# Optimization experiments

Hardware: AMD Instinct MI355X
Metric: run time of the kernel (lower is better)

Reference implementation:

```python
import jax, jax.numpy as jnp
import numpy as np
import math

D_MODEL = 1024
N_HEAD = 16
D_HEAD = D_MODEL // N_HEAD  # 64
D_KMAP = 128
B, L = 4, 4096


def setup_inputs() -> dict:
    key = jax.random.key(0)
    ks = jax.random.split(key, 10)
    s = 1.0 / math.sqrt(D_MODEL)
    inp = {
        "x": jax.random.normal(ks[0], (B, L, D_MODEL), dtype=jnp.float32),
        "proj_mat": jax.random.normal(ks[1], (D_HEAD, D_KMAP), dtype=jnp.float32),
        "Wq": jax.random.uniform(ks[2], (D_MODEL, D_MODEL), minval=-s, maxval=s),
        "bq": jax.random.uniform(ks[3], (D_MODEL,), minval=-s, maxval=s),
        "Wk": jax.random.uniform(ks[4], (D_MODEL, D_MODEL), minval=-s, maxval=s),
        "bk": jax.random.uniform(ks[5], (D_MODEL,), minval=-s, maxval=s),
        "Wv": jax.random.uniform(ks[6], (D_MODEL, D_MODEL), minval=-s, maxval=s),
        "bv": jax.random.uniform(ks[7], (D_MODEL,), minval=-s, maxval=s),
        "Wo": jax.random.uniform(ks[8], (D_MODEL, D_MODEL), minval=-s, maxval=s),
        "bo": jax.random.uniform(ks[9], (D_MODEL,), minval=-s, maxval=s),
    }
    return inp


def _fourier_kernel(x, proj_mat):
    # x: [B,L,H,d_head] -> [B,L,H,2*d_kmap]
    p = jnp.einsum("blhd,dm->blhm", x, proj_mat) / math.sqrt(D_HEAD)
    return jnp.concatenate([jnp.cos(p), jnp.sin(p)], axis=-1) / math.sqrt(D_KMAP)


def reference(x, proj_mat, Wq, bq, Wk, bk, Wv, bv, Wo, bo):
    Bv, Lv, _ = x.shape
    q = (x @ Wq.T + bq).reshape(Bv, Lv, N_HEAD, D_HEAD)
    k = (x @ Wk.T + bk).reshape(Bv, Lv, N_HEAD, D_HEAD)
    v = (x @ Wv.T + bv).reshape(Bv, Lv, N_HEAD, D_HEAD)
    q_prime = _fourier_kernel(q, proj_mat)  # [B,L,H,2M]
    k_prime = _fourier_kernel(k, proj_mat)  # [B,L,H,2M]
    kv = jnp.einsum("blhm,blhd->bhmd", k_prime, v)  # [B,H,2M,d_head]
    out = jnp.einsum("blhm,bhmd->blhd", q_prime, kv)  # [B,L,H,d_head]
    out = out.reshape(Bv, Lv, D_MODEL)
    return out @ Wo.T + bo
```

## Files before the change

kernel.cpp:

```cpp
#include <hip/hip_runtime.h>
#include <cstddef>
#include <cstdint>


typedef __attribute__((ext_vector_type(8))) short s8v;
typedef __attribute__((ext_vector_type(4))) short s4v;
typedef __attribute__((ext_vector_type(4))) float f32x4;

#define MFMA_BF16(a, b, c) __builtin_amdgcn_mfma_f32_16x16x32_bf16((a), (b), (c), 0, 0, 0)

#define P_SCALE 0.125f
#define F_SCALE 0.08838834764831845f

static __device__ __forceinline__ unsigned short f2bf(float f) {
  unsigned int u = __float_as_uint(f);
  u += 0x7fffu + ((u >> 16) & 1u);
  return (unsigned short)(u >> 16);
}

static __device__ __forceinline__ void gload_lds16(const void* g, void* l) {
  __builtin_amdgcn_global_load_lds(
      (const __attribute__((address_space(1))) unsigned int*)g,
      (__attribute__((address_space(3))) unsigned int*)l, 16, 0, 0);
}

__global__ void conv_all_kernel(const float* __restrict__ x,
                                const float* __restrict__ Wq, const float* __restrict__ Wk,
                                const float* __restrict__ Wv, const float* __restrict__ Wo,
                                const float* __restrict__ proj,
                                short* __restrict__ xb, short* __restrict__ Wqkvb,
                                short* __restrict__ Wob, short* __restrict__ projT) {
  const int bid = blockIdx.x;
  const int t = threadIdx.x;
  if (bid < 16384) {
    int i4 = (bid * 256 + t) * 4;
    float4 f = *(const float4*)(x + i4);
    s4v v;
    v[0] = (short)f2bf(f.x); v[1] = (short)f2bf(f.y);
    v[2] = (short)f2bf(f.z); v[3] = (short)f2bf(f.w);
    *(s4v*)(xb + i4) = v;
  } else if (bid < 20480) {
    int wi = (bid - 16384) >> 10;
    int lb = (bid - 16384) & 1023;
    const float* src = (wi == 0) ? Wq : (wi == 1) ? Wk : (wi == 2) ? Wv : Wo;
    short* dst = (wi < 3) ? (Wqkvb + (size_t)wi * 1048576) : Wob;
    int i4 = (lb * 256 + t) * 4;
    float4 f = *(const float4*)(src + i4);
    s4v v;
    v[0] = (short)f2bf(f.x); v[1] = (short)f2bf(f.y);
    v[2] = (short)f2bf(f.z); v[3] = (short)f2bf(f.w);
    *(s4v*)(dst + i4) = v;
  } else {
#pragma unroll
    for (int i = 0; i < 32; ++i) {
      int idx = t + i * 256;
      int d = idx >> 7, m = idx & 127;
      projT[m * 64 + d] = (short)f2bf(proj[idx]);
    }
  }
}

__global__ void qkv_gemm_kernel(const short* __restrict__ xb,
                                const short* __restrict__ Wqkv,
                                const float* __restrict__ bq_, const float* __restrict__ bk_,
                                const float* __restrict__ bv_,
                                short* __restrict__ qb, short* __restrict__ kb,
                                short* __restrict__ vT) {
  __shared__ __align__(16) short smem[17408];
  short* Al = smem;
  short* Bl = smem + 8192;

  const int t = threadIdx.x;
  const int bm = blockIdx.x, bn = blockIdx.y;
  const int row0 = bm * 128, n0 = bn * 128;
  const int lane = t & 63, w = t >> 6;
  const int wm = w & 1, wn = w >> 1;
  const int l15 = lane & 15, lq = lane >> 4;
  const int sx = (l15 & 7) * 8;

  f32x4 acc[4][4];
#pragma unroll
  for (int i = 0; i < 4; ++i)
#pragma unroll
    for (int j = 0; j < 4; ++j) acc[i][j] = (f32x4){0.f, 0.f, 0.f, 0.f};

  for (int k0 = 0; k0 < 1024; k0 += 64) {
#pragma unroll
    for (int i = 0; i < 4; ++i) {
      int c = t + i * 256;
      int r = c >> 3, cl = c & 7;
      int cg = cl ^ (r & 7);
      gload_lds16(xb   + (size_t)(row0 + r) * 1024 + k0 + cg * 8, Al + c * 8);
      gload_lds16(Wqkv + (size_t)(n0 + r) * 1024 + k0 + cg * 8, Bl + c * 8);
    }
    __syncthreads();
#pragma unroll
    for (int ks = 0; ks < 2; ++ks) {
      const int kb8 = (ks * 4 + lq) * 8;
      s8v af[4], bfr[4];
#pragma unroll
      for (int i = 0; i < 4; ++i)
        af[i] = *(s8v*)&Al[(wm * 64 + i * 16 + l15) * 64 + (kb8 ^ sx)];
#pragma unroll
      for (int j = 0; j < 4; ++j)
        bfr[j] = *(s8v*)&Bl[(wn * 64 + j * 16 + l15) * 64 + (kb8 ^ sx)];
#pragma unroll
      for (int i = 0; i < 4; ++i)
#pragma unroll
        for (int j = 0; j < 4; ++j)
          acc[i][j] = MFMA_BF16(af[i], bfr[j], acc[i][j]);
    }
    __syncthreads();
  }

  const int region = bn >> 3;
  if (region < 2) {
    const float* bias = (region == 0) ? bq_ : bk_;
    short* IM = smem;
#pragma unroll
    for (int j = 0; j < 4; ++j) {
      int cl = wn * 64 + j * 16 + l15;
      float bsv = bias[(n0 & 1023) + cl];
#pragma unroll
      for (int i = 0; i < 4; ++i)
#pragma unroll
        for (int r = 0; r < 4; ++r)
          IM[(wm * 64 + i * 16 + lq * 4 + r) * 136 + cl] = (short)f2bf(acc[i][j][r] + bsv);
    }
    __syncthreads();
    short* dst = (region == 0) ? qb : kb;
#pragma unroll
    for (int i = 0; i < 8; ++i) {
      int c = t + i * 256;
      int r = c >> 4, cc = c & 15;
      *(s8v*)&dst[(size_t)(row0 + r) * 1024 + (n0 & 1023) + cc * 8] =
          *(s8v*)&IM[r * 136 + cc * 8];
    }
  } else {
    short* IM = smem;
#pragma unroll
    for (int j = 0; j < 4; ++j) {
      int cl = wn * 64 + j * 16 + l15;
      float bsv = bv_[(n0 - 2048) + cl];
#pragma unroll
      for (int i = 0; i < 4; ++i) {
        s4v pk;
#pragma unroll
        for (int r = 0; r < 4; ++r) pk[r] = (short)f2bf(acc[i][j][r] + bsv);
        *(s4v*)&IM[cl * 136 + wm * 64 + i * 16 + lq * 4] = pk;
      }
    }
    __syncthreads();
    const int b = row0 >> 12;
    const int l0 = (bm & 31) * 128;
#pragma unroll
    for (int i = 0; i < 8; ++i) {
      int c = t + i * 256;
      int ci = c >> 4, cc = c & 15;
      int cv = (bn - 16) * 128 + ci;
      int grow = (b * 16 + (cv >> 6)) * 64 + (cv & 63);
      *(s8v*)&vT[(size_t)grow * 4096 + l0 + cc * 8] = *(s8v*)&IM[ci * 136 + cc * 8];
    }
  }
}

__global__ void kv_accum_kernel(const short* __restrict__ kb, const short* __restrict__ vT,
                                const short* __restrict__ projT, float* __restrict__ kv) {
  __shared__ __align__(16) short smem[26624];
  short* kt = smem;
  short* vt = smem + 4096;
  short* kpT = smem + 8192;

  const int t = threadIdx.x;
  const int bid = blockIdx.x;
  const int chunk = bid & 7, h = (bid >> 3) & 15, b = bid >> 7;
  const int lane = t & 63, w = t >> 6;
  const int l15 = lane & 15, lq = lane >> 4;
  const int sx = (l15 & 7) * 8;

  s8v pf[8][2];
#pragma unroll
  for (int nt = 0; nt < 8; ++nt)
#pragma unroll
    for (int ks = 0; ks < 2; ++ks)
      pf[nt][ks] = *(const s8v*)(projT + (size_t)(nt * 16 + l15) * 64 + ks * 32 + lq * 8);

  f32x4 kvacc[4][4];
#pragma unroll
  for (int i = 0; i < 4; ++i)
#pragma unroll
    for (int j = 0; j < 4; ++j) kvacc[i][j] = (f32x4){0.f, 0.f, 0.f, 0.f};

  for (int s = 0; s < 8; ++s) {
    const int l0s = chunk * 512 + s * 64;
#pragma unroll
    for (int i = 0; i < 2; ++i) {
      int c = t + i * 256;
      int r = c >> 3, cl = c & 7;
      int cg = cl ^ (r & 7);
      gload_lds16(kb + (size_t)(b * 4096 + l0s + r) * 1024 + h * 64 + cg * 8, kt + c * 8);
      gload_lds16(vT + (size_t)((b * 16 + h) * 64 + r) * 4096 + l0s + cg * 8, vt + c * 8);
    }
    __syncthreads();

    f32x4 pacc[8];
#pragma unroll
    for (int nt = 0; nt < 8; ++nt) pacc[nt] = (f32x4){0.f, 0.f, 0.f, 0.f};
#pragma unroll
    for (int ks = 0; ks < 2; ++ks) {
      const int kb8 = (ks * 4 + lq) * 8;
      s8v af = *(s8v*)&kt[(w * 16 + l15) * 64 + (kb8 ^ sx)];
#pragma unroll
      for (int nt = 0; nt < 8; ++nt) pacc[nt] = MFMA_BF16(af, pf[nt][ks], pacc[nt]);
    }
#pragma unroll
    for (int nt = 0; nt < 8; ++nt) {
      s4v cp, sp;
#pragma unroll
      for (int r = 0; r < 4; ++r) {
        float p = pacc[nt][r] * P_SCALE;
        float sv, cv;
        __sincosf(p, &sv, &cv);
        cp[r] = (short)f2bf(cv * F_SCALE);
        sp[r] = (short)f2bf(sv * F_SCALE);
      }
      int m = nt * 16 + l15;
      int rbase = w * 16 + lq * 4;
      *(s4v*)&kpT[m * 72 + rbase] = cp;
      *(s4v*)&kpT[(m + 128) * 72 + rbase] = sp;
    }
    __syncthreads();

#pragma unroll
    for (int ks = 0; ks < 2; ++ks) {
      const int kb8 = (ks * 4 + lq) * 8;
      s8v af[4], bf4[4];
#pragma unroll
      for (int i = 0; i < 4; ++i)
        af[i] = *(s8v*)&kpT[(w * 64 + i * 16 + l15) * 72 + ks * 32 + lq * 8];
#pragma unroll
      for (int j = 0; j < 4; ++j)
        bf4[j] = *(s8v*)&vt[(j * 16 + l15) * 64 + (kb8 ^ sx)];
#pragma unroll
      for (int i = 0; i < 4; ++i)
#pragma unroll
        for (int j = 0; j < 4; ++j)
          kvacc[i][j] = MFMA_BF16(af[i], bf4[j], kvacc[i][j]);
    }
    __syncthreads();
  }

  float* kvb = kv + (size_t)chunk * 1048576 + ((size_t)(b * 16 + h) << 14);
#pragma unroll
  for (int i = 0; i < 4; ++i)
#pragma unroll
    for (int j = 0; j < 4; ++j)
#pragma unroll
      for (int r = 0; r < 4; ++r) {
        int m = w * 64 + i * 16 + lq * 4 + r;
        int d = j * 16 + l15;
        kvb[(size_t)m * 64 + d] = kvacc[i][j][r];
      }
}

__global__ void kvT_kernel(const float* __restrict__ kvp, short* __restrict__ kvT) {
  __shared__ __align__(16) short im[4608];
  const int t = threadIdx.x;
  const int bh = blockIdx.x, mc = blockIdx.y;
  const float* base = kvp + (size_t)bh * 16384 + (size_t)mc * 4096;
#pragma unroll
  for (int i = 0; i < 4; ++i) {
    int idx4 = t + i * 256;
    int mm = idx4 >> 4, d4 = (idx4 & 15) * 4;
    float4 s = {0.f, 0.f, 0.f, 0.f};
#pragma unroll
    for (int c = 0; c < 8; ++c) {
      float4 v = *(const float4*)(base + (size_t)c * 1048576 + mm * 64 + d4);
      s.x += v.x; s.y += v.y; s.z += v.z; s.w += v.w;
    }
    im[(d4 + 0) * 72 + mm] = (short)f2bf(s.x);
    im[(d4 + 1) * 72 + mm] = (short)f2bf(s.y);
    im[(d4 + 2) * 72 + mm] = (short)f2bf(s.z);
    im[(d4 + 3) * 72 + mm] = (short)f2bf(s.w);
  }
  __syncthreads();
#pragma unroll
  for (int i = 0; i < 2; ++i) {
    int c = t + i * 256;
    int d = c >> 3, mm8 = (c & 7) * 8;
    *(s8v*)&kvT[(size_t)(bh * 64 + d) * 256 + mc * 64 + mm8] = *(s8v*)&im[d * 72 + mm8];
  }
}

__global__ void attn_kernel(const short* __restrict__ qb, const short* __restrict__ projT,
                            const short* __restrict__ kvT, short* __restrict__ attnb) {
  __shared__ __align__(16) short smem[12800];
  short* qt = smem;
  short* qA = smem + 4096;

  const int t = threadIdx.x;
  const int rt = blockIdx.x, h = blockIdx.y;
  const int row0 = rt * 64;
  const int b = row0 >> 12;
  const int lane = t & 63, w = t >> 6;
  const int l15 = lane & 15, lq = lane >> 4;
  const int sx = (l15 & 7) * 8;

  s8v pf[8][2];
#pragma unroll
  for (int nt = 0; nt < 8; ++nt)
#pragma unroll
    for (int ks = 0; ks < 2; ++ks)
      pf[nt][ks] = *(const s8v*)(projT + (size_t)(nt * 16 + l15) * 64 + ks * 32 + lq * 8);

#pragma unroll
  for (int i = 0; i < 2; ++i) {
    int c = t + i * 256;
    int r = c >> 3, cl = c & 7;
    int cg = cl ^ (r & 7);
    gload_lds16(qb + (size_t)(row0 + r) * 1024 + h * 64 + cg * 8, qt + c * 8);
  }
  __syncthreads();

  f32x4 pacc[8];
#pragma unroll
  for (int nt = 0; nt < 8; ++nt) pacc[nt] = (f32x4){0.f, 0.f, 0.f, 0.f};
#pragma unroll
  for (int ks = 0; ks < 2; ++ks) {
    const int kb8 = (ks * 4 + lq) * 8;
    s8v af = *(s8v*)&qt[(w * 16 + l15) * 64 + (kb8 ^ sx)];
#pragma unroll
    for (int nt = 0; nt < 8; ++nt) pacc[nt] = MFMA_BF16(af, pf[nt][ks], pacc[nt]);
  }

  const short* kvbase = kvT + ((size_t)(b * 16 + h) * 64) * 256;

  f32x4 aacc[4];
#pragma unroll
  for (int j = 0; j < 4; ++j) aacc[j] = (f32x4){0.f, 0.f, 0.f, 0.f};

#pragma unroll
  for (int half = 0; half < 2; ++half) {
#pragma unroll
    for (int nt = 0; nt < 8; ++nt)
#pragma unroll
      for (int r = 0; r < 4; ++r) {
        float p = pacc[nt][r] * P_SCALE;
        float fv = (half == 0) ? __cosf(p) : __sinf(p);
        qA[(w * 16 + lq * 4 + r) * 136 + nt * 16 + l15] = (short)f2bf(fv * F_SCALE);
      }
#pragma unroll
    for (int ks = 0; ks < 4; ++ks) {
      s8v af = *(s8v*)&qA[(w * 16 + l15) * 136 + ks * 32 + lq * 8];
#pragma unroll
      for (int j = 0; j < 4; ++j) {
        s8v bf4 = *(const s8v*)&kvbase[(size_t)(j * 16 + l15) * 256 + half * 128 +
                                       (ks * 4 + lq) * 8];
        aacc[j] = MFMA_BF16(af, bf4, aacc[j]);
      }
    }
  }

  __syncthreads();
#pragma unroll
  for (int j = 0; j < 4; ++j)
#pragma unroll
    for (int r = 0; r < 4; ++r)
      smem[(w * 16 + lq * 4 + r) * 72 + j * 16 + l15] = (short)f2bf(aacc[j][r]);
  __syncthreads();
#pragma unroll
  for (int i = 0; i < 2; ++i) {
    int c = t + i * 256;
    int r = c >> 3, cc = c & 7;
    *(s8v*)&attnb[(size_t)(row0 + r) * 1024 + h * 64 + cc * 8] = *(s8v*)&smem[r * 72 + cc * 8];
  }
}

__global__ void out_gemm_kernel(const short* __restrict__ attnb, const short* __restrict__ Wob,
                                const float* __restrict__ bo_, float* __restrict__ out) {
  __shared__ __align__(16) short smem[16384];
  short* Al = smem;
  short* Bl = smem + 8192;

  const int t = threadIdx.x;
  const int bm = blockIdx.x, bn = blockIdx.y;
  const int row0 = bm * 128, n0 = bn * 128;
  const int lane = t & 63, w = t >> 6;
  const int wm = w & 1, wn = w >> 1;
  const int l15 = lane & 15, lq = lane >> 4;
  const int sx = (l15 & 7) * 8;

  f32x4 acc[4][4];
#pragma unroll
  for (int i = 0; i < 4; ++i)
#pragma unroll
    for (int j = 0; j < 4; ++j) acc[i][j] = (f32x4){0.f, 0.f, 0.f, 0.f};

  for (int k0 = 0; k0 < 1024; k0 += 64) {
#pragma unroll
    for (int i = 0; i < 4; ++i) {
      int c = t + i * 256;
      int r = c >> 3, cl = c & 7;
      int cg = cl ^ (r & 7);
      gload_lds16(attnb + (size_t)(row0 + r) * 1024 + k0 + cg * 8, Al + c * 8);
      gload_lds16(Wob   + (size_t)(n0 + r) * 1024 + k0 + cg * 8, Bl + c * 8);
    }
    __syncthreads();
#pragma unroll
    for (int ks = 0; ks < 2; ++ks) {
      const int kb8 = (ks * 4 + lq) * 8;
      s8v af[4], bfr[4];
#pragma unroll
      for (int i = 0; i < 4; ++i)
        af[i] = *(s8v*)&Al[(wm * 64 + i * 16 + l15) * 64 + (kb8 ^ sx)];
#pragma unroll
      for (int j = 0; j < 4; ++j)
        bfr[j] = *(s8v*)&Bl[(wn * 64 + j * 16 + l15) * 64 + (kb8 ^ sx)];
#pragma unroll
      for (int i = 0; i < 4; ++i)
#pragma unroll
        for (int j = 0; j < 4; ++j)
          acc[i][j] = MFMA_BF16(af[i], bfr[j], acc[i][j]);
    }
    __syncthreads();
  }

#pragma unroll
  for (int j = 0; j < 4; ++j) {
    int cl = wn * 64 + j * 16 + l15;
    float bsv = bo_[n0 + cl];
#pragma unroll
    for (int i = 0; i < 4; ++i)
#pragma unroll
      for (int r = 0; r < 4; ++r)
        out[(size_t)(row0 + wm * 64 + i * 16 + lq * 4 + r) * 1024 + n0 + cl] =
            acc[i][j][r] + bsv;
  }
}

extern "C" void kernel_launch(void* const* d_in, const int* in_sizes, int n_in,
                              void* d_out, int out_size, void* d_ws, size_t ws_size,
                              hipStream_t stream) {
  const float* x    = (const float*)d_in[0];
  const float* proj = (const float*)d_in[1];
  const float* Wq   = (const float*)d_in[2];
  const float* bq   = (const float*)d_in[3];
  const float* Wk   = (const float*)d_in[4];
  const float* bk   = (const float*)d_in[5];
  const float* Wv   = (const float*)d_in[6];
  const float* bv   = (const float*)d_in[7];
  const float* Wo   = (const float*)d_in[8];
  const float* bo   = (const float*)d_in[9];
  float* out = (float*)d_out;

  char* wsb = (char*)d_ws;
  short* qb    = (short*)(wsb + 0);
  short* kb    = (short*)(wsb + 33554432);
  short* vT    = (short*)(wsb + 67108864);
  short* xb    = (short*)(wsb + 100663296);
  short* Wqkvb = (short*)(wsb + 134217728);
  short* Wob   = (short*)(wsb + 140509184);
  short* projT = (short*)(wsb + 142606336);
  float* kv_part = (float*)(wsb + 100663296);
  short* attnb = kb;
  short* kvT   = vT;

  conv_all_kernel<<<dim3(20481), dim3(256), 0, stream>>>(
      x, Wq, Wk, Wv, Wo, proj, xb, Wqkvb, Wob, projT);

  qkv_gemm_kernel<<<dim3(128, 24), dim3(256), 0, stream>>>(xb, Wqkvb, bq, bk, bv, qb, kb, vT);
  kv_accum_kernel<<<dim3(512), dim3(256), 0, stream>>>(kb, vT, projT, kv_part);
  kvT_kernel<<<dim3(64, 4), dim3(256), 0, stream>>>(kv_part, kvT);
  attn_kernel<<<dim3(256, 16), dim3(256), 0, stream>>>(qb, projT, kvT, attnb);
  out_gemm_kernel<<<dim3(128, 8), dim3(256), 0, stream>>>(attnb, Wob, bo, out);
}
```

Before: 445.1 us.

## Rewrite QKV GEMM as 256x256 double-buffered pipeline and stage kv in LDS

The QKV projection GEMM moves from 128x128 tiles with 256 threads to 256x256 tiles with 512 threads. It double-buffers LDS and splits each K step into four quadrant phases that prefetch the next tile during MFMA work, using explicit vmcnt waits, raw barriers and setprio. This is meant to raise arithmetic intensity and hide global-load latency. The attention kernel now stages the per-head kvT slice into swizzled LDS with global_load_lds instead of reading it directly from global memory per MFMA. The costs are 128KB of LDS per GEMM block, which limits occupancy, and hand-managed synchronization that is fragile.

```diff
diff --git a/kernel.cpp b/kernel.cpp
--- a/kernel.cpp
+++ b/kernel.cpp
@@ -60,108 +60,164 @@
   }
 }
 
-__global__ void qkv_gemm_kernel(const short* __restrict__ xb,
-                                const short* __restrict__ Wqkv,
-                                const float* __restrict__ bq_, const float* __restrict__ bk_,
-                                const float* __restrict__ bv_,
-                                short* __restrict__ qb, short* __restrict__ kb,
-                                short* __restrict__ vT) {
-  __shared__ __align__(16) short smem[17408];
-  short* Al = smem;
-  short* Bl = smem + 8192;
+__global__ __launch_bounds__(512, 2) void qkv_gemm256_kernel(
+    const short* __restrict__ xb, const short* __restrict__ Wqkv,
+    const float* __restrict__ bq_, const float* __restrict__ bk_,
+    const float* __restrict__ bv_,
+    short* __restrict__ qb, short* __restrict__ kb, short* __restrict__ vT) {
+  __shared__ __align__(16) short sm[65536];
 
   const int t = threadIdx.x;
   const int bm = blockIdx.x, bn = blockIdx.y;
-  const int row0 = bm * 128, n0 = bn * 128;
+  const int row0 = bm * 256, n0 = bn * 256;
   const int lane = t & 63, w = t >> 6;
-  const int wm = w & 1, wn = w >> 1;
+  const int wr = w >> 2, wc = w & 3;
   const int l15 = lane & 15, lq = lane >> 4;
   const int sx = (l15 & 7) * 8;
 
-  f32x4 acc[4][4];
-#pragma unroll
-  for (int i = 0; i < 4; ++i)
-#pragma unroll
-    for (int j = 0; j < 4; ++j) acc[i][j] = (f32x4){0.f, 0.f, 0.f, 0.f};
-
-  for (int k0 = 0; k0 < 1024; k0 += 64) {
-#pragma unroll
-    for (int i = 0; i < 4; ++i) {
-      int c = t + i * 256;
-      int r = c >> 3, cl = c & 7;
-      int cg = cl ^ (r & 7);
-      gload_lds16(xb   + (size_t)(row0 + r) * 1024 + k0 + cg * 8, Al + c * 8);
-      gload_lds16(Wqkv + (size_t)(n0 + r) * 1024 + k0 + cg * 8, Bl + c * 8);
-    }
-    __syncthreads();
-#pragma unroll
-    for (int ks = 0; ks < 2; ++ks) {
-      const int kb8 = (ks * 4 + lq) * 8;
-      s8v af[4], bfr[4];
-#pragma unroll
-      for (int i = 0; i < 4; ++i)
-        af[i] = *(s8v*)&Al[(wm * 64 + i * 16 + l15) * 64 + (kb8 ^ sx)];
-#pragma unroll
-      for (int j = 0; j < 4; ++j)
-        bfr[j] = *(s8v*)&Bl[(wn * 64 + j * 16 + l15) * 64 + (kb8 ^ sx)];
-#pragma unroll
-      for (int i = 0; i < 4; ++i)
-#pragma unroll
-        for (int j = 0; j < 4; ++j)
-          acc[i][j] = MFMA_BF16(af[i], bfr[j], acc[i][j]);
-    }
-    __syncthreads();
-  }
-
-  const int region = bn >> 3;
+  f32x4 acc[4][4][2];
+#pragma unroll
+  for (int q = 0; q < 4; ++q)
+#pragma unroll
+    for (int i = 0; i < 4; ++i)
+#pragma unroll
+      for (int j = 0; j < 2; ++j) acc[q][i][j] = (f32x4){0.f, 0.f, 0.f, 0.f};
+
+#define STAGE_A(mh, k0v, pp) {                                                  \
+    short* dsth = sm + (pp) * 32768 + (mh) * 8192;                              \
+    _Pragma("unroll") for (int ii = 0; ii < 2; ++ii) {                          \
+      int c = t + ii * 512; int r = c >> 3, cl = c & 7, cg = cl ^ (r & 7);      \
+      gload_lds16(xb + (size_t)(row0 + (mh) * 128 + r) * 1024 + (k0v) + cg * 8, \
+                  dsth + c * 8);                                                \
+    } }
+#define STAGE_B(nh, k0v, pp) {                                                  \
+    short* dsth = sm + (pp) * 32768 + 16384 + (nh) * 8192;                      \
+    _Pragma("unroll") for (int ii = 0; ii < 2; ++ii) {                          \
+      int c = t + ii * 512; int r = c >> 3, cl = c & 7, cg = cl ^ (r & 7);      \
+      gload_lds16(Wqkv + (size_t)(n0 + (nh) * 128 + r) * 1024 + (k0v) + cg * 8, \
+                  dsth + c * 8);                                                \
+    } }
+#define VM4 asm volatile("s_waitcnt vmcnt(4)" ::: "memory")
+#define VM0 asm volatile("s_waitcnt vmcnt(0)" ::: "memory")
+
+#define PHASE(mh, nh, STAGE_STMT, WAIT_STMT, SYNC) {                            \
+    const short* Ah = sm + p * 32768 + (mh) * 8192;                             \
+    const short* Bh = sm + p * 32768 + 16384 + (nh) * 8192;                     \
+    s8v af[4][2], bfr[2][2];                                                    \
+    _Pragma("unroll") for (int i = 0; i < 4; ++i)                               \
+      _Pragma("unroll") for (int ks = 0; ks < 2; ++ks)                          \
+        af[i][ks] = *(const s8v*)&Ah[(wr * 64 + i * 16 + l15) * 64 +            \
+                                     (((ks * 4 + lq) * 8) ^ sx)];               \
+    _Pragma("unroll") for (int j = 0; j < 2; ++j)                               \
+      _Pragma("unroll") for (int ks = 0; ks < 2; ++ks)                          \
+        bfr[j][ks] = *(const s8v*)&Bh[(wc * 32 + j * 16 + l15) * 64 +           \
+                                      (((ks * 4 + lq) * 8) ^ sx)];              \
+    STAGE_STMT;                                                                 \
+    WAIT_STMT;                                                                  \
+    if (SYNC) __builtin_amdgcn_s_barrier();                                     \
+    asm volatile("s_waitcnt lgkmcnt(0)" ::: "memory");                          \
+    __builtin_amdgcn_s_setprio(1);                                              \
+    _Pragma("unroll") for (int ks = 0; ks < 2; ++ks)                            \
+      _Pragma("unroll") for (int i = 0; i < 4; ++i)                             \
+        _Pragma("unroll") for (int j = 0; j < 2; ++j)                           \
+          acc[(mh) * 2 + (nh)][i][j] =                                          \
+              MFMA_BF16(af[i][ks], bfr[j][ks], acc[(mh) * 2 + (nh)][i][j]);     \
+    __builtin_amdgcn_s_setprio(0);                                              \
+    if (SYNC) __builtin_amdgcn_s_barrier();                                     \
+  }
+
+  STAGE_A(0, 0, 0);
+  STAGE_B(0, 0, 0);
+  STAGE_B(1, 0, 0);
+  STAGE_A(1, 0, 0);
+  VM4;
+  __builtin_amdgcn_s_barrier();
+
+  int p = 0;
+  for (int tt = 0; tt < 15; ++tt) {
+    const int k1 = (tt + 1) * 64;
+    PHASE(0, 0, STAGE_A(0, k1, p ^ 1), VM4, 1);
+    PHASE(0, 1, STAGE_B(0, k1, p ^ 1), VM4, 1);
+    PHASE(1, 0, STAGE_B(1, k1, p ^ 1), { }, 1);
+    PHASE(1, 1, STAGE_A(1, k1, p ^ 1), VM4, 1);
+    p ^= 1;
+  }
+  VM0;
+  __builtin_amdgcn_s_barrier();
+  PHASE(0, 0, { }, { }, 0);
+  PHASE(0, 1, { }, { }, 0);
+  PHASE(1, 0, { }, { }, 0);
+  PHASE(1, 1, { }, { }, 0);
+
+  __builtin_amdgcn_s_barrier();
+  short* im = sm;
+  const int region = bn >> 2;
   if (region < 2) {
     const float* bias = (region == 0) ? bq_ : bk_;
-    short* IM = smem;
-#pragma unroll
-    for (int j = 0; j < 4; ++j) {
-      int cl = wn * 64 + j * 16 + l15;
-      float bsv = bias[(n0 & 1023) + cl];
-#pragma unroll
-      for (int i = 0; i < 4; ++i)
-#pragma unroll
-        for (int r = 0; r < 4; ++r)
-          IM[(wm * 64 + i * 16 + lq * 4 + r) * 136 + cl] = (short)f2bf(acc[i][j][r] + bsv);
-    }
-    __syncthreads();
     short* dst = (region == 0) ? qb : kb;
-#pragma unroll
-    for (int i = 0; i < 8; ++i) {
-      int c = t + i * 256;
-      int r = c >> 4, cc = c & 15;
-      *(s8v*)&dst[(size_t)(row0 + r) * 1024 + (n0 & 1023) + cc * 8] =
-          *(s8v*)&IM[r * 136 + cc * 8];
+    const int cb = (bn & 3) * 256;
+#pragma unroll
+    for (int mh = 0; mh < 2; ++mh) {
+#pragma unroll
+      for (int nh = 0; nh < 2; ++nh)
+#pragma unroll
+        for (int j = 0; j < 2; ++j) {
+          int cl = nh * 128 + wc * 32 + j * 16 + l15;
+          float bsv = bias[cb + cl];
+#pragma unroll
+          for (int i = 0; i < 4; ++i)
+#pragma unroll
+            for (int r = 0; r < 4; ++r)
+              im[(wr * 64 + i * 16 + lq * 4 + r) * 264 + cl] =
+                  (short)f2bf(acc[mh * 2 + nh][i][j][r] + bsv);
+        }
+      __builtin_amdgcn_s_barrier();
+#pragma unroll
+      for (int i = 0; i < 8; ++i) {
+        int c = t + i * 512;
+        int r = c >> 5, cc = c & 31;
+        *(s8v*)&dst[(size_t)(row0 + mh * 128 + r) * 1024 + cb + cc * 8] =
+            *(s8v*)&im[r * 264 + cc * 8];
+      }
+      __builtin_amdgcn_s_barrier();
     }
   } else {
-    short* IM = smem;
-#pragma unroll
-    for (int j = 0; j < 4; ++j) {
-      int cl = wn * 64 + j * 16 + l15;
-      float bsv = bv_[(n0 - 2048) + cl];
-#pragma unroll
-      for (int i = 0; i < 4; ++i) {
-        s4v pk;
-#pragma unroll
-        for (int r = 0; r < 4; ++r) pk[r] = (short)f2bf(acc[i][j][r] + bsv);
-        *(s4v*)&IM[cl * 136 + wm * 64 + i * 16 + lq * 4] = pk;
+    const int b = bm >> 4;
+    const int l0 = (bm & 15) * 256;
+#pragma unroll
+    for (int nh = 0; nh < 2; ++nh) {
+#pragma unroll
+      for (int mh = 0; mh < 2; ++mh)
+#pragma unroll
+        for (int j = 0; j < 2; ++j) {
+          int cl = wc * 32 + j * 16 + l15;
+          float bsv = bv_[(bn - 8) * 256 + nh * 128 + cl];
+#pragma unroll
+          for (int i = 0; i < 4; ++i) {
+            s4v pk;
+#pragma unroll
+            for (int r = 0; r < 4; ++r)
+              pk[r] = (short)f2bf(acc[mh * 2 + nh][i][j][r] + bsv);
+            *(s4v*)&im[cl * 264 + mh * 128 + wr * 64 + i * 16 + lq * 4] = pk;
+          }
+        }
+      __builtin_amdgcn_s_barrier();
+#pragma unroll
+      for (int i = 0; i < 8; ++i) {
+        int c = t + i * 512;
+        int cp = c >> 5, rr8 = (c & 31) * 8;
+        int cv = (bn - 8) * 256 + nh * 128 + cp;
+        int grow = (b * 16 + (cv >> 6)) * 64 + (cv & 63);
+        *(s8v*)&vT[(size_t)grow * 4096 + l0 + rr8] = *(s8v*)&im[cp * 264 + rr8];
       }
-    }
-    __syncthreads();
-    const int b = row0 >> 12;
-    const int l0 = (bm & 31) * 128;
-#pragma unroll
-    for (int i = 0; i < 8; ++i) {
-      int c = t + i * 256;
-      int ci = c >> 4, cc = c & 15;
-      int cv = (bn - 16) * 128 + ci;
-      int grow = (b * 16 + (cv >> 6)) * 64 + (cv & 63);
-      *(s8v*)&vT[(size_t)grow * 4096 + l0 + cc * 8] = *(s8v*)&IM[ci * 136 + cc * 8];
-    }
-  }
+      __builtin_amdgcn_s_barrier();
+    }
+  }
+#undef STAGE_A
+#undef STAGE_B
+#undef VM4
+#undef VM0
+#undef PHASE
 }
 
 __global__ void kv_accum_kernel(const short* __restrict__ kb, const short* __restrict__ vT,
@@ -218,9 +274,9 @@
       s4v cp, sp;
 #pragma unroll
       for (int r = 0; r < 4; ++r) {
-        float p = pacc[nt][r] * P_SCALE;
+        float pv = pacc[nt][r] * P_SCALE;
         float sv, cv;
-        __sincosf(p, &sv, &cv);
+        __sincosf(pv, &sv, &cv);
         cp[r] = (short)f2bf(cv * F_SCALE);
         sp[r] = (short)f2bf(sv * F_SCALE);
       }
@@ -294,9 +350,10 @@
 
 __global__ void attn_kernel(const short* __restrict__ qb, const short* __restrict__ projT,
                             const short* __restrict__ kvT, short* __restrict__ attnb) {
-  __shared__ __align__(16) short smem[12800];
+  __shared__ __align__(16) short smem[20992];
   short* qt = smem;
   short* qA = smem + 4096;
+  short* kvt = smem + 12800;
 
   const int t = threadIdx.x;
   const int rt = blockIdx.x, h = blockIdx.y;
@@ -333,8 +390,6 @@
     for (int nt = 0; nt < 8; ++nt) pacc[nt] = MFMA_BF16(af, pf[nt][ks], pacc[nt]);
   }
 
-  const short* kvbase = kvT + ((size_t)(b * 16 + h) * 64) * 256;
-
   f32x4 aacc[4];
 #pragma unroll
   for (int j = 0; j < 4; ++j) aacc[j] = (f32x4){0.f, 0.f, 0.f, 0.f};
@@ -350,18 +405,27 @@
         qA[(w * 16 + lq * 4 + r) * 136 + nt * 16 + l15] = (short)f2bf(fv * F_SCALE);
       }
 #pragma unroll
+    for (int i = 0; i < 4; ++i) {
+      int c = t + i * 256;
+      int d = c >> 4, cl = c & 15;
+      int cg = cl ^ (d & 15);
+      gload_lds16(kvT + (size_t)((b * 16 + h) * 64 + d) * 256 + half * 128 + cg * 8,
+                  kvt + c * 8);
+    }
+    __syncthreads();
+#pragma unroll
     for (int ks = 0; ks < 4; ++ks) {
       s8v af = *(s8v*)&qA[(w * 16 + l15) * 136 + ks * 32 + lq * 8];
 #pragma unroll
       for (int j = 0; j < 4; ++j) {
-        s8v bf4 = *(const s8v*)&kvbase[(size_t)(j * 16 + l15) * 256 + half * 128 +
-                                       (ks * 4 + lq) * 8];
+        int row = j * 16 + l15;
+        s8v bf4 = *(s8v*)&kvt[row * 128 + (((ks * 4 + lq) ^ l15) * 8)];
         aacc[j] = MFMA_BF16(af, bf4, aacc[j]);
       }
     }
-  }
-
-  __syncthreads();
+    __syncthreads();
+  }
+
 #pragma unroll
   for (int j = 0; j < 4; ++j)
 #pragma unroll
@@ -468,7 +532,8 @@
   conv_all_kernel<<<dim3(20481), dim3(256), 0, stream>>>(
       x, Wq, Wk, Wv, Wo, proj, xb, Wqkvb, Wob, projT);
 
-  qkv_gemm_kernel<<<dim3(128, 24), dim3(256), 0, stream>>>(xb, Wqkvb, bq, bk, bv, qb, kb, vT);
+  qkv_gemm256_kernel<<<dim3(64, 12), dim3(512), 0, stream>>>(
+      xb, Wqkvb, bq, bk, bv, qb, kb, vT);
   kv_accum_kernel<<<dim3(512), dim3(256), 0, stream>>>(kb, vT, projT, kv_part);
   kvT_kernel<<<dim3(64, 4), dim3(256), 0, stream>>>(kv_part, kvT);
   attn_kernel<<<dim3(256, 16), dim3(256), 0, stream>>>(qb, projT, kvT, attnb);
```

Measured after the change: 417.8 us. -6.1%, faster.
